# Kernel tuning notes

Hardware: AMD Instinct MI355X
Metric: run time of the kernel (lower is better)

Reference implementation:

```python
import jax, jax.numpy as jnp
import numpy as np

B, F, H, D, K = 16384, 4096, 512, 64, 512  # batch, feat, hidden, emb_dim, codebook size
M = H // D  # code positions per sample


def _leaky(h):
    return jnp.where(h > 0, h, 0.01 * h)


def setup_inputs() -> dict:
    key = jax.random.key(0)
    ks = jax.random.split(key, 16)
    lin = lambda k, i, o: jax.random.normal(k, (i, o), jnp.float32) * (1.0 / np.sqrt(i))
    return {
        "x": jax.random.uniform(ks[0], (B, F), jnp.float32),
        "We1": lin(ks[1], F, 256), "be1": jnp.zeros((256,), jnp.float32),
        "We2": lin(ks[2], 256, 128), "be2": jnp.zeros((128,), jnp.float32),
        "We3": lin(ks[3], 128, H), "be3": jnp.zeros((H,), jnp.float32),
        "Wd1": lin(ks[4], H, 128), "bd1": jnp.zeros((128,), jnp.float32),
        "Wd2": lin(ks[5], 128, 256), "bd2": jnp.zeros((256,), jnp.float32),
        "Wd3": lin(ks[6], 256, F), "bd3": jnp.zeros((F,), jnp.float32),
        "codebook": jax.random.normal(ks[7], (D, K), jnp.float32) * 0.02,  # (emb_dim, num_embeddings)
    }


def _nearest(z_e, codebook):
    # z_e: (B, D, M); codebook: (D, K). Squared-distance argmin over K.
    x2 = jnp.sum(z_e * z_e, axis=1)                       # (B, M)
    xw = jnp.einsum('bdm,dk->bmk', z_e, codebook)         # (B, M, K)
    w2 = jnp.sum(codebook * codebook, axis=0)             # (K,)
    idx = jnp.argmin(x2[..., None] - 2.0 * xw + w2, axis=-1)  # (B, M)
    quant = jnp.swapaxes(codebook.T[idx], 1, 2)           # (B, D, M)
    return quant, idx


def reference(x, We1, be1, We2, be2, We3, be3, Wd1, bd1, Wd2, bd2, Wd3, bd3, codebook):
    # encoder MLP
    h = _leaky(x @ We1 + be1)
    h = _leaky(h @ We2 + be2)
    h = _leaky(h @ We3 + be3)                             # (B, H)
    z_e = h.reshape(B, D, M)
    # emb(z_e, weight_sg=True): straight-through, weight detached
    quant_sg, idx = _nearest(z_e, jax.lax.stop_gradient(codebook))
    z_q = z_e + jax.lax.stop_gradient(quant_sg - z_e)
    # emb(z_e.detach()): grads (if any) flow to codebook via gather
    emb, _ = _nearest(jax.lax.stop_gradient(z_e), codebook)
    # decoder MLP
    g = _leaky(z_q.reshape(B, H) @ Wd1 + bd1)
    g = _leaky(g @ Wd2 + bd2)
    X_pred = jax.nn.sigmoid(g @ Wd3 + bd3)                # (B, F)
    return idx, z_e, z_q, emb, X_pred
```

## Files before the change

kernel.cpp:

```cpp
#include <hip/hip_runtime.h>
#include <cstdint>
#include <cstddef>


static constexpr int BB = 16384;

typedef __attribute__((ext_vector_type(8))) short short8;
typedef __attribute__((ext_vector_type(8))) _Float16 half8;
typedef __attribute__((ext_vector_type(4))) float f32x4;

__device__ __forceinline__ unsigned short f2bf(float f) {
    union { float f; uint32_t u; } v; v.f = f;
    uint32_t r = (v.u + 0x7FFFu + ((v.u >> 16) & 1u)) >> 16;
    return (unsigned short)r;
}

__device__ __forceinline__ void lds_barrier() {
    asm volatile("s_waitcnt lgkmcnt(0)" ::: "memory");
    __builtin_amdgcn_s_barrier();
    __builtin_amdgcn_sched_barrier(0);
}

__global__ __launch_bounds__(256) void combine_act(
    const float* __restrict__ part, int S, size_t MN,
    const float* __restrict__ bias, int N,
    float* __restrict__ outF)
{
    const size_t e = ((size_t)blockIdx.x * 256 + threadIdx.x) * 4;
    if (e >= MN) return;
    float4 s = *(const float4*)(part + e);
    for (int i = 1; i < S; i++) {
        const float4 p = *(const float4*)(part + (size_t)i * MN + e);
        s.x += p.x; s.y += p.y; s.z += p.z; s.w += p.w;
    }
    const int col = (int)(e & (size_t)(N - 1));
    const float4 bv = *(const float4*)(bias + col);
    float v0 = s.x + bv.x, v1 = s.y + bv.y, v2 = s.z + bv.z, v3 = s.w + bv.w;
    v0 = (v0 > 0.f) ? v0 : 0.01f * v0;
    v1 = (v1 > 0.f) ? v1 : 0.01f * v1;
    v2 = (v2 > 0.f) ? v2 : 0.01f * v2;
    v3 = (v3 > 0.f) ? v3 : 0.01f * v3;
    float4 o; o.x = v0; o.y = v1; o.z = v2; o.w = v3;
    *(float4*)(outF + e) = o;
}

__global__ __launch_bounds__(256) void transpose_cast(
    const float* __restrict__ W, unsigned short* __restrict__ WT, int R, int Cc)
{
    __shared__ float s[32][33];
    const int tx = threadIdx.x & 31, ty = threadIdx.x >> 5;
    const int c0 = blockIdx.x * 32, r0 = blockIdx.y * 32;
#pragma unroll
    for (int i = 0; i < 4; i++)
        s[ty + i * 8][tx] = W[(size_t)(r0 + ty + i * 8) * Cc + c0 + tx];
    __syncthreads();
#pragma unroll
    for (int i = 0; i < 4; i++)
        WT[(size_t)(c0 + ty + i * 8) * R + r0 + tx] = f2bf(s[tx][ty + i * 8]);
}

__global__ __launch_bounds__(256) void transpose_split_f16(
    const float* __restrict__ W, unsigned short* __restrict__ Th,
    unsigned short* __restrict__ Tl, int R, int Cc)
{
    __shared__ float s[32][33];
    const int tx = threadIdx.x & 31, ty = threadIdx.x >> 5;
    const int c0 = blockIdx.x * 32, r0 = blockIdx.y * 32;
#pragma unroll
    for (int i = 0; i < 4; i++)
        s[ty + i * 8][tx] = W[(size_t)(r0 + ty + i * 8) * Cc + c0 + tx];
    __syncthreads();
#pragma unroll
    for (int i = 0; i < 4; i++) {
        const float f = s[tx][ty + i * 8];
        const _Float16 h = (_Float16)f;
        const float fh = (float)h;
        const _Float16 lo = (_Float16)((f - fh) * 4096.0f);
        union { _Float16 hf; unsigned short u; } ch, cl;
        ch.hf = h; cl.hf = lo;
        Th[(size_t)(c0 + ty + i * 8) * R + r0 + tx] = ch.u;
        Tl[(size_t)(c0 + ty + i * 8) * R + r0 + tx] = cl.u;
    }
}

__global__ __launch_bounds__(512) void cb_w2(
    const float* __restrict__ cb, float* __restrict__ w2g)
{
    const int k = threadIdx.x;
    float s = 0.f;
    for (int d = 0; d < 64; d++) { float c = cb[d * 512 + k]; s = fmaf(c, c, s); }
    w2g[k] = s;
}

static constexpr int E1KS = 1024;

template<int BUF>
__device__ __forceinline__ void enc1_step(
    int K0,
    const float* __restrict__ gA,
    const unsigned short* __restrict__ gBh,
    const unsigned short* __restrict__ gBl,
    short (&Ah)[2][2048], short (&Al)[2][2048],
    half8 (&bhC)[4], half8 (&bhN)[4], half8 (&blS)[4],
    f32x4& p0, f32x4& p1, f32x4& q0, f32x4& q1,
    f32x4 (&acc1)[4][4], f32x4 (&acc2)[4][4],
    int aoff, int fr0)
{
    constexpr size_t rstep = (size_t)16 * 4096;
    const int kn1 = K0 + 32, kn3 = K0 + 96;
    lds_barrier();
#pragma unroll
    for (int j = 0; j < 4; j++)
        blS[j] = *(const half8*)(gBl + (size_t)j * rstep + K0);
    if (kn1 < E1KS) {
#pragma unroll
        for (int j = 0; j < 4; j++)
            bhN[j] = *(const half8*)(gBh + (size_t)j * rstep + kn1);
    }
    f32x4 f0, f1;
    if (kn3 < E1KS) {
        f0 = __builtin_nontemporal_load((const f32x4*)(gA + kn3));
        f1 = __builtin_nontemporal_load((const f32x4*)(gA + kn3 + 4));
    }
    half8 ah[4];
#pragma unroll
    for (int i = 0; i < 4; i++)
        ah[i] = *(const half8*)&Ah[BUF][(i << 9) + fr0];
#pragma unroll
    for (int i = 0; i < 4; i++)
#pragma unroll
        for (int j = 0; j < 4; j++)
            acc1[i][j] = __builtin_amdgcn_mfma_f32_16x16x32_f16(
                ah[i], bhC[j], acc1[i][j], 0, 0, 0);
#pragma unroll
    for (int i = 0; i < 4; i++)
#pragma unroll
        for (int j = 0; j < 4; j++)
            acc2[i][j] = __builtin_amdgcn_mfma_f32_16x16x32_f16(
                ah[i], blS[j], acc2[i][j], 0, 0, 0);
    half8 al[4];
#pragma unroll
    for (int i = 0; i < 4; i++)
        al[i] = *(const half8*)&Al[BUF][(i << 9) + fr0];
#pragma unroll
    for (int i = 0; i < 4; i++)
#pragma unroll
        for (int j = 0; j < 4; j++)
            acc2[i][j] = __builtin_amdgcn_mfma_f32_16x16x32_f16(
                al[i], bhC[j], acc2[i][j], 0, 0, 0);
    if (kn1 < E1KS) {
        float fv[8];
        *(f32x4*)&fv[0] = p0;
        *(f32x4*)&fv[4] = p1;
        union { _Float16 h[8]; short8 s; } uh, ul;
#pragma unroll
        for (int e = 0; e < 8; e++) {
            const float f = fv[e];
            const _Float16 h = (_Float16)f;
            const float fh = (float)h;
            uh.h[e] = h;
            ul.h[e] = (_Float16)((f - fh) * 4096.0f);
        }
        *(short8*)&Ah[BUF ^ 1][aoff] = uh.s;
        *(short8*)&Al[BUF ^ 1][aoff] = ul.s;
    }
    p0 = q0; p1 = q1;
    if (kn3 < E1KS) { q0 = f0; q1 = f1; }
}

__global__ __launch_bounds__(256, 2) void gemm_f16x2_enc1(
    const float* __restrict__ X,
    const unsigned short* __restrict__ Bh,
    const unsigned short* __restrict__ Bl,
    float* __restrict__ part)
{
    __shared__ short Ah[2][2048];
    __shared__ short Al[2][2048];
    const int tid = threadIdx.x;
    const int l = tid & 63, w = tid >> 6;
    const int lm = l & 15, lq = l >> 4;
    const int bm = blockIdx.y * 64;
    const int kStart = blockIdx.z * E1KS;

    const float* gA = X + (size_t)(bm + w * 16 + lm) * 4096 + kStart + lq * 8;
    const unsigned short* gBh = Bh + (size_t)(w * 64 + lm) * 4096 + kStart + lq * 8;
    const unsigned short* gBl = Bl + (size_t)(w * 64 + lm) * 4096 + kStart + lq * 8;
    constexpr size_t rstep = (size_t)16 * 4096;

    const int aoff = (w << 9) + (l << 3);
    const int fr0 = (lq << 7) + (lm << 3);

    f32x4 acc1[4][4], acc2[4][4];
#pragma unroll
    for (int i = 0; i < 4; i++)
#pragma unroll
        for (int j = 0; j < 4; j++) {
            acc1[i][j] = (f32x4){0.f, 0.f, 0.f, 0.f};
            acc2[i][j] = (f32x4){0.f, 0.f, 0.f, 0.f};
        }

    half8 bhA[4], bhB[4], blS[4];
    f32x4 p0, p1, q0, q1;

    {
#pragma unroll
        for (int j = 0; j < 4; j++)
            bhA[j] = *(const half8*)(gBh + (size_t)j * rstep);
        f32x4 a0 = __builtin_nontemporal_load((const f32x4*)(gA));
        f32x4 a1 = __builtin_nontemporal_load((const f32x4*)(gA + 4));
        p0 = __builtin_nontemporal_load((const f32x4*)(gA + 32));
        p1 = __builtin_nontemporal_load((const f32x4*)(gA + 36));
        q0 = __builtin_nontemporal_load((const f32x4*)(gA + 64));
        q1 = __builtin_nontemporal_load((const f32x4*)(gA + 68));
        float fv[8];
        *(f32x4*)&fv[0] = a0;
        *(f32x4*)&fv[4] = a1;
        union { _Float16 h[8]; short8 s; } uh, ul;
#pragma unroll
        for (int e = 0; e < 8; e++) {
            const float f = fv[e];
            const _Float16 h = (_Float16)f;
            const float fh = (float)h;
            uh.h[e] = h;
            ul.h[e] = (_Float16)((f - fh) * 4096.0f);
        }
        *(short8*)&Ah[0][aoff] = uh.s;
        *(short8*)&Al[0][aoff] = ul.s;
    }

    for (int k2 = 0; k2 < E1KS; k2 += 64) {
        enc1_step<0>(k2,      gA, gBh, gBl, Ah, Al, bhA, bhB, blS,
                     p0, p1, q0, q1, acc1, acc2, aoff, fr0);
        enc1_step<1>(k2 + 32, gA, gBh, gBl, Ah, Al, bhB, bhA, blS,
                     p0, p1, q0, q1, acc1, acc2, aoff, fr0);
    }

    float* P = part + (size_t)blockIdx.z * BB * 256;
    const float inv = 0.000244140625f;
#pragma unroll
    for (int i = 0; i < 4; i++)
#pragma unroll
        for (int j = 0; j < 4; j++) {
            const int col = w * 64 + j * 16 + lm;
#pragma unroll
            for (int r = 0; r < 4; r++) {
                const int row = bm + i * 16 + lq * 4 + r;
                P[(size_t)row * 256 + col] = acc1[i][j][r] + inv * acc2[i][j][r];
            }
        }
}

template<int BUF, int NJ, int KLEN>
__device__ __forceinline__ void mid_step(
    int K0,
    const float* __restrict__ gA,
    const unsigned short* __restrict__ gBh,
    const unsigned short* __restrict__ gBl,
    short (&Ah)[2][2048], short (&Al)[2][2048],
    half8 (&bhC)[NJ], half8 (&bhN)[NJ], half8 (&blS)[NJ],
    f32x4& p0, f32x4& p1,
    f32x4 (&acc1)[4][NJ], f32x4 (&acc2)[4][NJ],
    int aoff, int fr0)
{
    constexpr size_t rstep = (size_t)16 * KLEN;
    const int kn1 = K0 + 32, kn2 = K0 + 64;
    lds_barrier();
#pragma unroll
    for (int j = 0; j < NJ; j++)
        blS[j] = *(const half8*)(gBl + (size_t)j * rstep + K0);
    if (kn1 < KLEN) {
#pragma unroll
        for (int j = 0; j < NJ; j++)
            bhN[j] = *(const half8*)(gBh + (size_t)j * rstep + kn1);
    }
    f32x4 f0, f1;
    if (kn2 < KLEN) {
        f0 = *(const f32x4*)(gA + kn2);
        f1 = *(const f32x4*)(gA + kn2 + 4);
    }
    half8 ah[4];
#pragma unroll
    for (int i = 0; i < 4; i++)
        ah[i] = *(const half8*)&Ah[BUF][(i << 9) + fr0];
#pragma unroll
    for (int i = 0; i < 4; i++)
#pragma unroll
        for (int j = 0; j < NJ; j++)
            acc1[i][j] = __builtin_amdgcn_mfma_f32_16x16x32_f16(
                ah[i], bhC[j], acc1[i][j], 0, 0, 0);
#pragma unroll
    for (int i = 0; i < 4; i++)
#pragma unroll
        for (int j = 0; j < NJ; j++)
            acc2[i][j] = __builtin_amdgcn_mfma_f32_16x16x32_f16(
                ah[i], blS[j], acc2[i][j], 0, 0, 0);
    half8 al[4];
#pragma unroll
    for (int i = 0; i < 4; i++)
        al[i] = *(const half8*)&Al[BUF][(i << 9) + fr0];
#pragma unroll
    for (int i = 0; i < 4; i++)
#pragma unroll
        for (int j = 0; j < NJ; j++)
            acc2[i][j] = __builtin_amdgcn_mfma_f32_16x16x32_f16(
                al[i], bhC[j], acc2[i][j], 0, 0, 0);
    if (kn1 < KLEN) {
        float fv[8];
        *(f32x4*)&fv[0] = p0;
        *(f32x4*)&fv[4] = p1;
        union { _Float16 h[8]; short8 s; } uh, ul;
#pragma unroll
        for (int e = 0; e < 8; e++) {
            const float f = fv[e];
            const _Float16 h = (_Float16)f;
            const float fh = (float)h;
            uh.h[e] = h;
            ul.h[e] = (_Float16)((f - fh) * 4096.0f);
        }
        *(short8*)&Ah[BUF ^ 1][aoff] = uh.s;
        *(short8*)&Al[BUF ^ 1][aoff] = ul.s;
    }
    if (kn2 < KLEN) { p0 = f0; p1 = f1; }
}

template<int NJ, int KLEN, int ACT>
__global__ __launch_bounds__(256, 2) void gemm_f16x2_mid(
    const float* __restrict__ A,
    const unsigned short* __restrict__ Bh,
    const unsigned short* __restrict__ Bl,
    const float* __restrict__ bias,
    float* __restrict__ Cf, unsigned short* __restrict__ Cb)
{
    __shared__ short Ah[2][2048];
    __shared__ short Al[2][2048];
    const int tid = threadIdx.x;
    const int l = tid & 63, w = tid >> 6;
    const int lm = l & 15, lq = l >> 4;
    const int bm = blockIdx.y * 64;
    const int bn = blockIdx.x * (64 * NJ);
    const int N = gridDim.x * 64 * NJ;

    const float* gA = A + (size_t)(bm + w * 16 + lm) * KLEN + lq * 8;
    const unsigned short* gBh = Bh + (size_t)(bn + w * (16 * NJ) + lm) * KLEN + lq * 8;
    const unsigned short* gBl = Bl + (size_t)(bn + w * (16 * NJ) + lm) * KLEN + lq * 8;
    constexpr size_t rstep = (size_t)16 * KLEN;

    const int aoff = (w << 9) + (l << 3);
    const int fr0 = (lq << 7) + (lm << 3);

    f32x4 acc1[4][NJ], acc2[4][NJ];
#pragma unroll
    for (int i = 0; i < 4; i++)
#pragma unroll
        for (int j = 0; j < NJ; j++) {
            acc1[i][j] = (f32x4){0.f, 0.f, 0.f, 0.f};
            acc2[i][j] = (f32x4){0.f, 0.f, 0.f, 0.f};
        }

    half8 bhA[NJ], bhB[NJ], blS[NJ];
    f32x4 p0, p1;

    {
#pragma unroll
        for (int j = 0; j < NJ; j++)
            bhA[j] = *(const half8*)(gBh + (size_t)j * rstep);
        f32x4 a0 = *(const f32x4*)(gA);
        f32x4 a1 = *(const f32x4*)(gA + 4);
        p0 = *(const f32x4*)(gA + 32);
        p1 = *(const f32x4*)(gA + 36);
        float fv[8];
        *(f32x4*)&fv[0] = a0;
        *(f32x4*)&fv[4] = a1;
        union { _Float16 h[8]; short8 s; } uh, ul;
#pragma unroll
        for (int e = 0; e < 8; e++) {
            const float f = fv[e];
            const _Float16 h = (_Float16)f;
            const float fh = (float)h;
            uh.h[e] = h;
            ul.h[e] = (_Float16)((f - fh) * 4096.0f);
        }
        *(short8*)&Ah[0][aoff] = uh.s;
        *(short8*)&Al[0][aoff] = ul.s;
    }

    for (int k2 = 0; k2 < KLEN; k2 += 64) {
        mid_step<0, NJ, KLEN>(k2,      gA, gBh, gBl, Ah, Al, bhA, bhB, blS,
                              p0, p1, acc1, acc2, aoff, fr0);
        mid_step<1, NJ, KLEN>(k2 + 32, gA, gBh, gBl, Ah, Al, bhB, bhA, blS,
                              p0, p1, acc1, acc2, aoff, fr0);
    }

    const float inv = 0.000244140625f;
#pragma unroll
    for (int i = 0; i < 4; i++)
#pragma unroll
        for (int j = 0; j < NJ; j++) {
            const int col = bn + w * (16 * NJ) + j * 16 + lm;
            const float bv = bias[col];
#pragma unroll
            for (int r = 0; r < 4; r++) {
                const int row = bm + i * 16 + lq * 4 + r;
                float v = acc1[i][j][r] + inv * acc2[i][j][r] + bv;
                v = (v > 0.f) ? v : 0.01f * v;
                if (ACT == 0) Cf[(size_t)row * N + col] = v;
                else          Cb[(size_t)row * N + col] = f2bf(v);
            }
        }
}

__device__ __forceinline__ void dec3_step(
    int kn,
    const unsigned short* __restrict__ gA,
    const unsigned short* __restrict__ gB,
    short8 (&afC)[4], short8 (&bfC)[4],
    short8 (&afN)[4], short8 (&bfN)[4],
    f32x4 (&acc)[4][4])
{
    if (kn < 256) {
#pragma unroll
        for (int i = 0; i < 4; i++)
            afN[i] = *(const short8*)(gA + (size_t)i * 16 * 256 + kn);
#pragma unroll
        for (int j = 0; j < 4; j++)
            bfN[j] = *(const short8*)(gB + (size_t)j * 16 * 256 + kn);
    }
#pragma unroll
    for (int i = 0; i < 4; i++)
#pragma unroll
        for (int j = 0; j < 4; j++)
            acc[i][j] = __builtin_amdgcn_mfma_f32_16x16x32_bf16(
                afC[i], bfC[j], acc[i][j], 0, 0, 0);
}

__global__ __launch_bounds__(256) void gemm_bf16_dec3(
    const unsigned short* __restrict__ Ag,
    const unsigned short* __restrict__ Bt,
    const float* __restrict__ bias, float* __restrict__ C)
{
    const int tid = threadIdx.x;
    const int l = tid & 63, w = tid >> 6;
    const int lm = l & 15, lq = l >> 4;
    const int bm = blockIdx.y * 128, bn = blockIdx.x * 128;
    const int wm = (w >> 1) * 64, wn = (w & 1) * 64;

    const unsigned short* gA = Ag + (size_t)(bm + wm + lm) * 256 + lq * 8;
    const unsigned short* gB = Bt + (size_t)(bn + wn + lm) * 256 + lq * 8;

    f32x4 acc[4][4];
#pragma unroll
    for (int i = 0; i < 4; i++)
#pragma unroll
        for (int j = 0; j < 4; j++) acc[i][j] = (f32x4){0.f, 0.f, 0.f, 0.f};

    short8 afA[4], afB[4], bfA[4], bfB[4];
#pragma unroll
    for (int i = 0; i < 4; i++)
        afA[i] = *(const short8*)(gA + (size_t)i * 16 * 256);
#pragma unroll
    for (int j = 0; j < 4; j++)
        bfA[j] = *(const short8*)(gB + (size_t)j * 16 * 256);

    for (int k0 = 0; k0 < 256; k0 += 64) {
        dec3_step(k0 + 32, gA, gB, afA, bfA, afB, bfB, acc);
        dec3_step(k0 + 64, gA, gB, afB, bfB, afA, bfA, acc);
    }

#pragma unroll
    for (int i = 0; i < 4; i++) {
#pragma unroll
        for (int j = 0; j < 4; j++) {
            const int col = bn + wn + j * 16 + lm;
            const float bv = bias[col];
#pragma unroll
            for (int r = 0; r < 4; r++) {
                const int row = bm + wm + i * 16 + lq * 4 + r;
                float v = acc[i][j][r] + bv;
                v = 1.0f / (1.0f + __expf(-v));
                C[(size_t)row * 4096 + col] = v;
            }
        }
    }
}

template<int CH>
__device__ __forceinline__ void vq_chunk(
    int w, int lm, int lq, int fr0,
    const short* Ahh, const short* All,
    const unsigned short* __restrict__ cbTh,
    const unsigned short* __restrict__ cbTl,
    const float* __restrict__ w2g,
    float (&bdv)[2][4], int (&bkv)[2][4])
{
    const unsigned short* gBh = cbTh + (size_t)(w * 128 + CH * 64 + lm) * 64 + lq * 8;
    const unsigned short* gBl = cbTl + (size_t)(w * 128 + CH * 64 + lm) * 64 + lq * 8;
    half8 bh0[4], bl0[4], bh1[4], bl1[4];
#pragma unroll
    for (int j = 0; j < 4; j++) {
        bh0[j] = *(const half8*)(gBh + (size_t)j * 1024);
        bl0[j] = *(const half8*)(gBl + (size_t)j * 1024);
        bh1[j] = *(const half8*)(gBh + (size_t)j * 1024 + 32);
        bl1[j] = *(const half8*)(gBl + (size_t)j * 1024 + 32);
    }
    half8 ah0[2], al0[2], ah1[2], al1[2];
#pragma unroll
    for (int i = 0; i < 2; i++) {
        ah0[i] = *(const half8*)&Ahh[i * 1024 + fr0];
        al0[i] = *(const half8*)&All[i * 1024 + fr0];
        ah1[i] = *(const half8*)&Ahh[i * 1024 + 512 + fr0];
        al1[i] = *(const half8*)&All[i * 1024 + 512 + fr0];
    }
    f32x4 acc1[2][4], acc2[2][4];
#pragma unroll
    for (int i = 0; i < 2; i++)
#pragma unroll
        for (int j = 0; j < 4; j++) {
            acc1[i][j] = (f32x4){0.f, 0.f, 0.f, 0.f};
            acc2[i][j] = (f32x4){0.f, 0.f, 0.f, 0.f};
        }
#pragma unroll
    for (int i = 0; i < 2; i++)
#pragma unroll
        for (int j = 0; j < 4; j++)
            acc1[i][j] = __builtin_amdgcn_mfma_f32_16x16x32_f16(
                ah0[i], bh0[j], acc1[i][j], 0, 0, 0);
#pragma unroll
    for (int i = 0; i < 2; i++)
#pragma unroll
        for (int j = 0; j < 4; j++)
            acc2[i][j] = __builtin_amdgcn_mfma_f32_16x16x32_f16(
                al0[i], bh0[j], acc2[i][j], 0, 0, 0);
#pragma unroll
    for (int i = 0; i < 2; i++)
#pragma unroll
        for (int j = 0; j < 4; j++)
            acc2[i][j] = __builtin_amdgcn_mfma_f32_16x16x32_f16(
                ah0[i], bl0[j], acc2[i][j], 0, 0, 0);
#pragma unroll
    for (int i = 0; i < 2; i++)
#pragma unroll
        for (int j = 0; j < 4; j++)
            acc1[i][j] = __builtin_amdgcn_mfma_f32_16x16x32_f16(
                ah1[i], bh1[j], acc1[i][j], 0, 0, 0);
#pragma unroll
    for (int i = 0; i < 2; i++)
#pragma unroll
        for (int j = 0; j < 4; j++)
            acc2[i][j] = __builtin_amdgcn_mfma_f32_16x16x32_f16(
                ah1[i], bl1[j], acc2[i][j], 0, 0, 0);
#pragma unroll
    for (int i = 0; i < 2; i++)
#pragma unroll
        for (int j = 0; j < 4; j++)
            acc2[i][j] = __builtin_amdgcn_mfma_f32_16x16x32_f16(
                al1[i], bh1[j], acc2[i][j], 0, 0, 0);

    const float inv = 0.000244140625f;
    float w2v[4];
#pragma unroll
    for (int j = 0; j < 4; j++) w2v[j] = w2g[w * 128 + CH * 64 + j * 16 + lm];
#pragma unroll
    for (int i = 0; i < 2; i++)
#pragma unroll
        for (int r = 0; r < 4; r++) {
            float bd = bdv[i][r]; int bk = bkv[i][r];
#pragma unroll
            for (int j = 0; j < 4; j++) {
                const float s = acc1[i][j][r] + inv * acc2[i][j][r];
                const float dsc = w2v[j] - 2.0f * s;
                const int kc = w * 128 + CH * 64 + j * 16 + lm;
                if (dsc < bd || (dsc == bd && kc < bk)) { bd = dsc; bk = kc; }
            }
            bdv[i][r] = bd; bkv[i][r] = bk;
        }
}

__global__ __launch_bounds__(256) void vq_mfma(
    const float* __restrict__ ze, const float* __restrict__ cb,
    const unsigned short* __restrict__ cbTh,
    const unsigned short* __restrict__ cbTl,
    const float* __restrict__ w2g,
    float* __restrict__ idxf, float* __restrict__ zq, float* __restrict__ emb)
{
    __shared__ short Ahh[2048], All[2048];
    __shared__ float As[64][33];
    __shared__ float redv[32][4];
    __shared__ int   redk[32][4];
    __shared__ int   kq[32];
    const int tid = threadIdx.x;
    const int l = tid & 63, w = tid >> 6;
    const int lm = l & 15, lq = l >> 4;
    const int b0 = blockIdx.x * 4;

#pragma unroll
    for (int ff = 0; ff < 2; ff++) {
        const int e = (tid + ff * 256) * 4;
        const int s = e >> 9, r = e & 511, d = r >> 3, m = r & 7;
        const f32x4 v = *(const f32x4*)(ze + (size_t)b0 * 512 + e);
#pragma unroll
        for (int c = 0; c < 4; c++) {
            const float fv = v[c];
            const int row = s * 8 + m + c;
            As[d][row] = fv;
            const _Float16 h = (_Float16)fv;
            const float fh = (float)h;
            const _Float16 lo = (_Float16)((fv - fh) * 4096.0f);
            union { _Float16 hf; unsigned short u; } ch, cl;
            ch.hf = h; cl.hf = lo;
            const int off = (row >> 4) * 1024 + (d >> 5) * 512 +
                            ((d >> 3) & 3) * 128 + (row & 15) * 8 + (d & 7);
            Ahh[off] = (short)ch.u;
            All[off] = (short)cl.u;
        }
    }
    __syncthreads();

    const int fr0 = lq * 128 + lm * 8;
    float bdv[2][4];
    int   bkv[2][4];
#pragma unroll
    for (int i = 0; i < 2; i++)
#pragma unroll
        for (int r = 0; r < 4; r++) { bdv[i][r] = 3.4e38f; bkv[i][r] = 1 << 30; }

    vq_chunk<0>(w, lm, lq, fr0, Ahh, All, cbTh, cbTl, w2g, bdv, bkv);
    vq_chunk<1>(w, lm, lq, fr0, Ahh, All, cbTh, cbTl, w2g, bdv, bkv);

#pragma unroll
    for (int i = 0; i < 2; i++)
#pragma unroll
        for (int r = 0; r < 4; r++) {
            float bd = bdv[i][r]; int bk = bkv[i][r];
#pragma unroll
            for (int off = 1; off < 16; off <<= 1) {
                const float od = __shfl_xor(bd, off);
                const int   ok = __shfl_xor(bk, off);
                if (od < bd || (od == bd && ok < bk)) { bd = od; bk = ok; }
            }
            if (lm == 0) {
                const int row = i * 16 + lq * 4 + r;
                redv[row][w] = bd;
                redk[row][w] = bk;
            }
        }
    __syncthreads();

    if (tid < 32) {
        float bd = redv[tid][0]; int bk = redk[tid][0];
#pragma unroll
        for (int ww = 1; ww < 4; ww++) {
            const float od = redv[tid][ww];
            const int   ok = redk[tid][ww];
            if (od < bd || (od == bd && ok < bk)) { bd = od; bk = ok; }
        }
        idxf[(size_t)b0 * 8 + tid] = (float)bk;
        kq[tid] = bk;
    }
    __syncthreads();

    {
        const int ss = tid >> 6, dd = tid & 63;
        float zq8[8], em8[8];
#pragma unroll
        for (int mm = 0; mm < 8; mm++) {
            const int k = kq[ss * 8 + mm];
            const float q = cb[dd * 512 + k];
            const float z = As[dd][ss * 8 + mm];
            em8[mm] = q;
            zq8[mm] = z + (q - z);
        }
        float* zqp = zq + (size_t)(b0 + ss) * 512 + dd * 8;
        float* emp = emb + (size_t)(b0 + ss) * 512 + dd * 8;
        *(float4*)zqp = *(float4*)&zq8[0];
        *(float4*)(zqp + 4) = *(float4*)&zq8[4];
        *(float4*)emp = *(float4*)&em8[0];
        *(float4*)(emp + 4) = *(float4*)&em8[4];
    }
}

extern "C" void kernel_launch(void* const* d_in, const int* in_sizes, int n_in,
                              void* d_out, int out_size, void* d_ws, size_t ws_size,
                              hipStream_t stream)
{
    const float* x   = (const float*)d_in[0];
    const float* We1 = (const float*)d_in[1];
    const float* be1 = (const float*)d_in[2];
    const float* We2 = (const float*)d_in[3];
    const float* be2 = (const float*)d_in[4];
    const float* We3 = (const float*)d_in[5];
    const float* be3 = (const float*)d_in[6];
    const float* Wd1 = (const float*)d_in[7];
    const float* bd1 = (const float*)d_in[8];
    const float* Wd2 = (const float*)d_in[9];
    const float* bd2 = (const float*)d_in[10];
    const float* Wd3 = (const float*)d_in[11];
    const float* bd3 = (const float*)d_in[12];
    const float* cb  = (const float*)d_in[13];

    float* out   = (float*)d_out;
    float* o_idx = out;
    float* o_ze  = o_idx + 131072;
    float* o_zq  = o_ze + 8388608;
    float* o_emb = o_zq + 8388608;
    float* o_X   = o_emb + 8388608;

    float* h1 = (float*)d_ws;
    float* h2 = h1 + (size_t)BB * 256;
    float* g1 = h1;
    unsigned short* g2b = (unsigned short*)(h1 + (size_t)BB * 128);
    unsigned short* WT  = (unsigned short*)h2;

    unsigned short* Bth  = (unsigned short*)(o_X + 16777216);
    unsigned short* Btl  = Bth + 1048576;
    unsigned short* W2h  = Btl + 1048576;
    unsigned short* W2l  = W2h + 32768;
    unsigned short* W3h  = W2l + 32768;
    unsigned short* W3l  = W3h + 65536;
    unsigned short* Wd1h = W3l + 65536;
    unsigned short* Wd1l = Wd1h + 65536;
    unsigned short* Wd2h = Wd1l + 65536;
    unsigned short* Wd2l = Wd2h + 32768;
    unsigned short* cbTh = Wd2l + 32768;
    unsigned short* cbTl = cbTh + 32768;
    float*          w2g  = (float*)(cbTl + 32768);

    transpose_split_f16<<<dim3(8, 128), 256, 0, stream>>>(We1, Bth, Btl, 4096, 256);
    transpose_split_f16<<<dim3(4, 8),   256, 0, stream>>>(We2, W2h, W2l, 256, 128);
    transpose_split_f16<<<dim3(16, 4),  256, 0, stream>>>(We3, W3h, W3l, 128, 512);
    transpose_split_f16<<<dim3(4, 16),  256, 0, stream>>>(Wd1, Wd1h, Wd1l, 512, 128);
    transpose_split_f16<<<dim3(8, 4),   256, 0, stream>>>(Wd2, Wd2h, Wd2l, 128, 256);
    transpose_split_f16<<<dim3(16, 2),  256, 0, stream>>>(cb, cbTh, cbTl, 64, 512);
    cb_w2<<<dim3(1), dim3(512), 0, stream>>>(cb, w2g);

    gemm_f16x2_enc1<<<dim3(1, 256, 4), 256, 0, stream>>>(x, Bth, Btl, o_X);
    combine_act<<<4096, 256, 0, stream>>>(o_X, 4, (size_t)BB * 256, be1, 256, h1);
    gemm_f16x2_mid<2, 256, 0><<<dim3(1, 256), 256, 0, stream>>>(
        h1, W2h, W2l, be2, h2, nullptr);
    gemm_f16x2_mid<4, 128, 0><<<dim3(2, 256), 256, 0, stream>>>(
        h2, W3h, W3l, be3, o_ze, nullptr);

    transpose_cast<<<dim3(128, 8), 256, 0, stream>>>(Wd3, WT, 256, 4096);

    vq_mfma<<<dim3(4096), dim3(256), 0, stream>>>(
        o_ze, cb, cbTh, cbTl, w2g, o_idx, o_zq, o_emb);

    gemm_f16x2_mid<2, 512, 0><<<dim3(1, 256), 256, 0, stream>>>(
        o_zq, Wd1h, Wd1l, bd1, g1, nullptr);
    gemm_f16x2_mid<4, 128, 1><<<dim3(1, 256), 256, 0, stream>>>(
        g1, Wd2h, Wd2l, bd2, nullptr, g2b);
    gemm_bf16_dec3<<<dim3(32, 128), 256, 0, stream>>>(g2b, WT, bd3, o_X);
}
```

Baseline: 968.1 us.

## Fuse split-K combine and activation into enc2 GEMM; merge prep kernels

```diff
diff --git a/kernel.cpp b/kernel.cpp
--- a/kernel.cpp
+++ b/kernel.cpp
@@ -21,29 +21,6 @@
     __builtin_amdgcn_sched_barrier(0);
 }
 
-__global__ __launch_bounds__(256) void combine_act(
-    const float* __restrict__ part, int S, size_t MN,
-    const float* __restrict__ bias, int N,
-    float* __restrict__ outF)
-{
-    const size_t e = ((size_t)blockIdx.x * 256 + threadIdx.x) * 4;
-    if (e >= MN) return;
-    float4 s = *(const float4*)(part + e);
-    for (int i = 1; i < S; i++) {
-        const float4 p = *(const float4*)(part + (size_t)i * MN + e);
-        s.x += p.x; s.y += p.y; s.z += p.z; s.w += p.w;
-    }
-    const int col = (int)(e & (size_t)(N - 1));
-    const float4 bv = *(const float4*)(bias + col);
-    float v0 = s.x + bv.x, v1 = s.y + bv.y, v2 = s.z + bv.z, v3 = s.w + bv.w;
-    v0 = (v0 > 0.f) ? v0 : 0.01f * v0;
-    v1 = (v1 > 0.f) ? v1 : 0.01f * v1;
-    v2 = (v2 > 0.f) ? v2 : 0.01f * v2;
-    v3 = (v3 > 0.f) ? v3 : 0.01f * v3;
-    float4 o; o.x = v0; o.y = v1; o.z = v2; o.w = v3;
-    *(float4*)(outF + e) = o;
-}
-
 __global__ __launch_bounds__(256) void transpose_cast(
     const float* __restrict__ W, unsigned short* __restrict__ WT, int R, int Cc)
 {
@@ -59,13 +36,13 @@
         WT[(size_t)(c0 + ty + i * 8) * R + r0 + tx] = f2bf(s[tx][ty + i * 8]);
 }
 
-__global__ __launch_bounds__(256) void transpose_split_f16(
+__device__ __forceinline__ void tsplit_blk(
     const float* __restrict__ W, unsigned short* __restrict__ Th,
-    unsigned short* __restrict__ Tl, int R, int Cc)
-{
-    __shared__ float s[32][33];
+    unsigned short* __restrict__ Tl, int R, int Cc, int bx, int by,
+    float (&s)[32][33])
+{
     const int tx = threadIdx.x & 31, ty = threadIdx.x >> 5;
-    const int c0 = blockIdx.x * 32, r0 = blockIdx.y * 32;
+    const int c0 = bx * 32, r0 = by * 32;
 #pragma unroll
     for (int i = 0; i < 4; i++)
         s[ty + i * 8][tx] = W[(size_t)(r0 + ty + i * 8) * Cc + c0 + tx];
@@ -83,13 +60,35 @@
     }
 }
 
-__global__ __launch_bounds__(512) void cb_w2(
-    const float* __restrict__ cb, float* __restrict__ w2g)
-{
-    const int k = threadIdx.x;
-    float s = 0.f;
-    for (int d = 0; d < 64; d++) { float c = cb[d * 512 + k]; s = fmaf(c, c, s); }
-    w2g[k] = s;
+__global__ __launch_bounds__(256) void prep_all(
+    const float* __restrict__ We1, unsigned short* __restrict__ B1h, unsigned short* __restrict__ B1l,
+    const float* __restrict__ We2, unsigned short* __restrict__ W2h, unsigned short* __restrict__ W2l,
+    const float* __restrict__ We3, unsigned short* __restrict__ W3h, unsigned short* __restrict__ W3l,
+    const float* __restrict__ Wd1, unsigned short* __restrict__ Wd1h, unsigned short* __restrict__ Wd1l,
+    const float* __restrict__ Wd2, unsigned short* __restrict__ Wd2h, unsigned short* __restrict__ Wd2l,
+    const float* __restrict__ cb,  unsigned short* __restrict__ cbTh, unsigned short* __restrict__ cbTl,
+    float* __restrict__ w2g)
+{
+    __shared__ float s[32][33];
+    const int b = blockIdx.x;
+    if (b < 1024) {
+        tsplit_blk(We1, B1h, B1l, 4096, 256, b & 7, b >> 3, s);
+    } else if (b < 1056) {
+        const int bb = b - 1024; tsplit_blk(We2, W2h, W2l, 256, 128, bb & 3, bb >> 2, s);
+    } else if (b < 1120) {
+        const int bb = b - 1056; tsplit_blk(We3, W3h, W3l, 128, 512, bb & 15, bb >> 4, s);
+    } else if (b < 1184) {
+        const int bb = b - 1120; tsplit_blk(Wd1, Wd1h, Wd1l, 512, 128, bb & 3, bb >> 2, s);
+    } else if (b < 1216) {
+        const int bb = b - 1184; tsplit_blk(Wd2, Wd2h, Wd2l, 128, 256, bb & 7, bb >> 3, s);
+    } else if (b < 1248) {
+        const int bb = b - 1216; tsplit_blk(cb, cbTh, cbTl, 64, 512, bb & 15, bb >> 4, s);
+    } else {
+        const int k = (b - 1248) * 256 + threadIdx.x;
+        float sm = 0.f;
+        for (int d = 0; d < 64; d++) { float c = cb[d * 512 + k]; sm = fmaf(c, c, sm); }
+        w2g[k] = sm;
+    }
 }
 
 static constexpr int E1KS = 1024;
@@ -246,6 +245,180 @@
             for (int r = 0; r < 4; r++) {
                 const int row = bm + i * 16 + lq * 4 + r;
                 P[(size_t)row * 256 + col] = acc1[i][j][r] + inv * acc2[i][j][r];
+            }
+        }
+}
+
+struct AQuad { f32x4 a0, b0, c0, d0, a1, b1, c1, d1; };
+
+__device__ __forceinline__ void enc2_convert(
+    const AQuad& P, const float* bias_s, int kabs,
+    short (&AhD)[2048], short (&AlD)[2048], int aoff)
+{
+    f32x4 s0 = ((P.a0 + P.b0) + P.c0) + P.d0;
+    f32x4 s1 = ((P.a1 + P.b1) + P.c1) + P.d1;
+    float fv[8];
+#pragma unroll
+    for (int c = 0; c < 4; c++) {
+        float v = s0[c] + bias_s[kabs + c];
+        fv[c] = (v > 0.f) ? v : 0.01f * v;
+    }
+#pragma unroll
+    for (int c = 0; c < 4; c++) {
+        float v = s1[c] + bias_s[kabs + 4 + c];
+        fv[4 + c] = (v > 0.f) ? v : 0.01f * v;
+    }
+    union { _Float16 h[8]; short8 s; } uh, ul;
+#pragma unroll
+    for (int e = 0; e < 8; e++) {
+        const float f = fv[e];
+        const _Float16 h = (_Float16)f;
+        const float fh = (float)h;
+        uh.h[e] = h;
+        ul.h[e] = (_Float16)((f - fh) * 4096.0f);
+    }
+    *(short8*)&AhD[aoff] = uh.s;
+    *(short8*)&AlD[aoff] = ul.s;
+}
+
+__device__ __forceinline__ void enc2_ldraw(AQuad& P, const float* g, size_t PS) {
+    P.a0 = *(const f32x4*)(g);
+    P.b0 = *(const f32x4*)(g + PS);
+    P.c0 = *(const f32x4*)(g + 2 * PS);
+    P.d0 = *(const f32x4*)(g + 3 * PS);
+    P.a1 = *(const f32x4*)(g + 4);
+    P.b1 = *(const f32x4*)(g + PS + 4);
+    P.c1 = *(const f32x4*)(g + 2 * PS + 4);
+    P.d1 = *(const f32x4*)(g + 3 * PS + 4);
+}
+
+template<int BUF>
+__device__ __forceinline__ void enc2_step(
+    int K0,
+    const float* __restrict__ gA, size_t PS,
+    const unsigned short* __restrict__ gBh,
+    const unsigned short* __restrict__ gBl,
+    short (&Ah)[2][2048], short (&Al)[2][2048],
+    half8 (&bhC)[2], half8 (&bhN)[2], half8 (&blS)[2],
+    AQuad& P, const float* bias_s, int kb,
+    f32x4 (&acc1)[4][2], f32x4 (&acc2)[4][2],
+    int aoff, int fr0)
+{
+    constexpr size_t rstep = (size_t)16 * 256;
+    const int kn1 = K0 + 32, kn2 = K0 + 64;
+    lds_barrier();
+#pragma unroll
+    for (int j = 0; j < 2; j++)
+        blS[j] = *(const half8*)(gBl + (size_t)j * rstep + K0);
+    if (kn1 < 256) {
+#pragma unroll
+        for (int j = 0; j < 2; j++)
+            bhN[j] = *(const half8*)(gBh + (size_t)j * rstep + kn1);
+    }
+    AQuad F;
+    if (kn2 < 256) enc2_ldraw(F, gA + kn2, PS);
+    half8 ah[4];
+#pragma unroll
+    for (int i = 0; i < 4; i++)
+        ah[i] = *(const half8*)&Ah[BUF][(i << 9) + fr0];
+#pragma unroll
+    for (int i = 0; i < 4; i++)
+#pragma unroll
+        for (int j = 0; j < 2; j++)
+            acc1[i][j] = __builtin_amdgcn_mfma_f32_16x16x32_f16(
+                ah[i], bhC[j], acc1[i][j], 0, 0, 0);
+#pragma unroll
+    for (int i = 0; i < 4; i++)
+#pragma unroll
+        for (int j = 0; j < 2; j++)
+            acc2[i][j] = __builtin_amdgcn_mfma_f32_16x16x32_f16(
+                ah[i], blS[j], acc2[i][j], 0, 0, 0);
+    half8 al[4];
+#pragma unroll
+    for (int i = 0; i < 4; i++)
+        al[i] = *(const half8*)&Al[BUF][(i << 9) + fr0];
+#pragma unroll
+    for (int i = 0; i < 4; i++)
+#pragma unroll
+        for (int j = 0; j < 2; j++)
+            acc2[i][j] = __builtin_amdgcn_mfma_f32_16x16x32_f16(
+                al[i], bhC[j], acc2[i][j], 0, 0, 0);
+    if (kn1 < 256)
+        enc2_convert(P, bias_s, kb + kn1, Ah[BUF ^ 1], Al[BUF ^ 1], aoff);
+    if (kn2 < 256) P = F;
+}
+
+__global__ __launch_bounds__(256, 2) void gemm_f16x2_enc2(
+    const float* __restrict__ part,
+    const unsigned short* __restrict__ Bh,
+    const unsigned short* __restrict__ Bl,
+    const float* __restrict__ be1,
+    const float* __restrict__ be2,
+    float* __restrict__ Cf)
+{
+    constexpr size_t PS = (size_t)BB * 256;
+    __shared__ short Ah[2][2048];
+    __shared__ short Al[2][2048];
+    __shared__ float bias_s[256];
+    const int tid = threadIdx.x;
+    const int l = tid & 63, w = tid >> 6;
+    const int lm = l & 15, lq = l >> 4;
+    const int bm = blockIdx.y * 64;
+
+    const float* gA = part + (size_t)(bm + w * 16 + lm) * 256 + lq * 8;
+    const unsigned short* gBh = Bh + (size_t)(w * 32 + lm) * 256 + lq * 8;
+    const unsigned short* gBl = Bl + (size_t)(w * 32 + lm) * 256 + lq * 8;
+    constexpr size_t rstep = (size_t)16 * 256;
+
+    const int aoff = (w << 9) + (l << 3);
+    const int fr0 = (lq << 7) + (lm << 3);
+    const int kb = lq * 8;
+
+    bias_s[tid] = be1[tid];
+    __syncthreads();
+
+    f32x4 acc1[4][2], acc2[4][2];
+#pragma unroll
+    for (int i = 0; i < 4; i++)
+#pragma unroll
+        for (int j = 0; j < 2; j++) {
+            acc1[i][j] = (f32x4){0.f, 0.f, 0.f, 0.f};
+            acc2[i][j] = (f32x4){0.f, 0.f, 0.f, 0.f};
+        }
+
+    half8 bhA[2], bhB[2], blS[2];
+    AQuad P;
+
+    {
+#pragma unroll
+        for (int j = 0; j < 2; j++)
+            bhA[j] = *(const half8*)(gBh + (size_t)j * rstep);
+        AQuad A0;
+        enc2_ldraw(A0, gA, PS);
+        enc2_ldraw(P, gA + 32, PS);
+        enc2_convert(A0, bias_s, kb, Ah[0], Al[0], aoff);
+    }
+
+    for (int k2 = 0; k2 < 256; k2 += 64) {
+        enc2_step<0>(k2,      gA, PS, gBh, gBl, Ah, Al, bhA, bhB, blS,
+                     P, bias_s, kb, acc1, acc2, aoff, fr0);
+        enc2_step<1>(k2 + 32, gA, PS, gBh, gBl, Ah, Al, bhB, bhA, blS,
+                     P, bias_s, kb, acc1, acc2, aoff, fr0);
+    }
+
+    const float inv = 0.000244140625f;
+#pragma unroll
+    for (int i = 0; i < 4; i++)
+#pragma unroll
+        for (int j = 0; j < 2; j++) {
+            const int col = w * 32 + j * 16 + lm;
+            const float bv = be2[col];
+#pragma unroll
+            for (int r = 0; r < 4; r++) {
+                const int row = bm + i * 16 + lq * 4 + r;
+                float v = acc1[i][j][r] + inv * acc2[i][j][r] + bv;
+                v = (v > 0.f) ? v : 0.01f * v;
+                Cf[(size_t)row * 128 + col] = v;
             }
         }
 }
@@ -724,24 +897,19 @@
     unsigned short* cbTl = cbTh + 32768;
     float*          w2g  = (float*)(cbTl + 32768);
 
-    transpose_split_f16<<<dim3(8, 128), 256, 0, stream>>>(We1, Bth, Btl, 4096, 256);
-    transpose_split_f16<<<dim3(4, 8),   256, 0, stream>>>(We2, W2h, W2l, 256, 128);
-    transpose_split_f16<<<dim3(16, 4),  256, 0, stream>>>(We3, W3h, W3l, 128, 512);
-    transpose_split_f16<<<dim3(4, 16),  256, 0, stream>>>(Wd1, Wd1h, Wd1l, 512, 128);
-    transpose_split_f16<<<dim3(8, 4),   256, 0, stream>>>(Wd2, Wd2h, Wd2l, 128, 256);
-    transpose_split_f16<<<dim3(16, 2),  256, 0, stream>>>(cb, cbTh, cbTl, 64, 512);
-    cb_w2<<<dim3(1), dim3(512), 0, stream>>>(cb, w2g);
+    prep_all<<<dim3(1250), 256, 0, stream>>>(
+        We1, Bth, Btl, We2, W2h, W2l, We3, W3h, W3l,
+        Wd1, Wd1h, Wd1l, Wd2, Wd2h, Wd2l, cb, cbTh, cbTl, w2g);
 
     gemm_f16x2_enc1<<<dim3(1, 256, 4), 256, 0, stream>>>(x, Bth, Btl, o_X);
-    combine_act<<<4096, 256, 0, stream>>>(o_X, 4, (size_t)BB * 256, be1, 256, h1);
-    gemm_f16x2_mid<2, 256, 0><<<dim3(1, 256), 256, 0, stream>>>(
-        h1, W2h, W2l, be2, h2, nullptr);
+    gemm_f16x2_enc2<<<dim3(1, 256), 256, 0, stream>>>(
+        o_X, W2h, W2l, be1, be2, h2);
     gemm_f16x2_mid<4, 128, 0><<<dim3(2, 256), 256, 0, stream>>>(
         h2, W3h, W3l, be3, o_ze, nullptr);
 
     transpose_cast<<<dim3(128, 8), 256, 0, stream>>>(Wd3, WT, 256, 4096);
 
-    vq_mfma<<<dim3(4096), dim3(256), 0, stream>>>(
+    vq_mfma<<<dim3(4096), 256, 0, stream>>>(
         o_ze, cb, cbTh, cbTl, w2g, o_idx, o_zq, o_emb);
 
     gemm_f16x2_mid<2, 512, 0><<<dim3(1, 256), 256, 0, stream>>>(
```

New measurement: 950.0 us. About the same (-1.9%).
